# Kernel optimization log

Hardware: AMD Instinct MI355X
Metric: run time of the kernel (lower is better)

## Reference

```python
import jax, jax.numpy as jnp
import numpy as np

EPS = 1e-5
K_UP = 5      # k_upsample
SCALE = 2

def _conv(x, w, pad):
    # NCHW conv, no bias
    return jax.lax.conv_general_dilated(
        x, w, window_strides=(1, 1), padding=((pad, pad), (pad, pad)),
        dimension_numbers=('NCHW', 'OIHW', 'NCHW'))

def _bn(x, gamma, beta):
    # train-mode BatchNorm2d forward: batch stats over (N,H,W), biased var
    m = x.mean(axis=(0, 2, 3), keepdims=True)
    v = x.var(axis=(0, 2, 3), keepdims=True)
    xn = (x - m) * jax.lax.rsqrt(v + EPS)
    return xn * gamma[None, :, None, None] + beta[None, :, None, None]

def _pixel_shuffle(x, r):
    b, c, h, w = x.shape
    co = c // (r * r)
    x = x.reshape(b, co, r, r, h, w)
    x = x.transpose(0, 1, 4, 2, 5, 3)  # b, co, h, r, w, r
    return x.reshape(b, co, h * r, w * r)

def setup_inputs() -> dict:
    key = jax.random.key(0)
    ks = jax.random.split(key, 3)
    b, c, h, w = 8, 128, 64, 64
    mid = 64
    return {
        'x': jax.random.normal(ks[0], (b, c, h, w), jnp.float32),
        'comp_w': jax.random.normal(ks[1], (mid, c, 1, 1), jnp.float32) * (1.0 / np.sqrt(c)),
        'comp_g': jnp.ones((mid,), jnp.float32),
        'comp_b': jnp.zeros((mid,), jnp.float32),
        'enc_w': jax.random.normal(ks[2], ((K_UP * SCALE) ** 2, mid, 3, 3), jnp.float32) * (1.0 / np.sqrt(mid * 9)),
        'enc_g': jnp.ones(((K_UP * SCALE) ** 2,), jnp.float32),
        'enc_b': jnp.zeros(((K_UP * SCALE) ** 2,), jnp.float32),
    }

def reference(x, comp_w, comp_g, comp_b, enc_w, enc_g, enc_b):
    b, c, h, w = x.shape
    hm, wm = h * SCALE, w * SCALE
    # --- kernel prediction branch ---
    t = jax.nn.silu(_bn(_conv(x, comp_w, 0), comp_g, comp_b))        # [b,64,h,w]
    t = _bn(_conv(t, enc_w, 1), enc_g, enc_b)                        # [b,100,h,w] (act=False)
    t = _pixel_shuffle(t, SCALE)                                     # [b,25,hm,wm]
    wgt = jax.nn.softmax(t, axis=1)                                  # [b,25,hm,wm]
    # --- feature reassembly branch ---
    x_up = jnp.repeat(jnp.repeat(x, SCALE, axis=2), SCALE, axis=3)   # nearest upsample
    pad = (K_UP // 2) * SCALE  # = 4, preserves hm x wm with dilation=SCALE
    xp = jnp.pad(x_up, ((0, 0), (0, 0), (pad, pad), (pad, pad)))
    # unfold: kernel K_UP, dilation SCALE -> [b, c, 25, hm, wm], taps in (kh, kw) order
    patches = jnp.stack(
        [xp[:, :, dy * SCALE:dy * SCALE + hm, dx * SCALE:dx * SCALE + wm]
         for dy in range(K_UP) for dx in range(K_UP)], axis=2)
    # content-aware weighted sum over the 25 taps
    return jnp.einsum('bkhw,bckhw->bchw', wgt, patches)
```

## Files before the change

kernel.cpp:

```cpp
#include <hip/hip_runtime.h>
#include <hip/hip_bf16.h>
#include <math.h>

#define C_   128
#define HW_  4096
#define OC_  100
#define NSTAT_ 32768.0f

typedef __bf16 bf16x8 __attribute__((ext_vector_type(8)));
typedef __bf16 bf16x4 __attribute__((ext_vector_type(4)));
typedef float  f32x4  __attribute__((ext_vector_type(4)));

__global__ __launch_bounds__(256, 4) void k_conv1(const float* __restrict__ x,
                                                  const float* __restrict__ w,
                                                  const float* __restrict__ wenc,
                                                  __bf16* __restrict__ t1c,
                                                  float* __restrict__ csum,
                                                  float* __restrict__ csq,
                                                  __bf16* __restrict__ wprep) {
    __shared__ __bf16 xt[64 * 128];
    __shared__ __bf16 wt[64 * 128];
    __shared__ float sS[64], sQ[64];

    int blk = blockIdx.x;
    int b = blk & 7;
    int chunk = blk >> 3;
    int px0 = chunk * 64;
    int tid = threadIdx.x;
    if (tid < 64) { sS[tid] = 0.f; sQ[tid] = 0.f; }

    if (blk < 63) {
#pragma unroll
        for (int u = 0; u < 4; ++u) {
            int idx = blk * 1024 + u * 256 + tid;
            int oc = idx / 576, k = idx - oc * 576;
            int tap = k >> 6, ic = k & 63;
            wprep[idx] = (oc < OC_) ? (__bf16)wenc[((size_t)oc * 64 + ic) * 9 + tap]
                                    : (__bf16)0.f;
        }
    }

#pragma unroll
    for (int it = 0; it < 8; ++it) {
        int j = it * 256 + tid;
        int oc = j >> 5, f = j & 31;
        float4 v = *(const float4*)(w + (size_t)oc * 128 + f * 4);
        int blki = (f >> 1) ^ (oc & 15);
        bf16x4 st;
        st[0] = (__bf16)v.x; st[1] = (__bf16)v.y; st[2] = (__bf16)v.z; st[3] = (__bf16)v.w;
        *(bf16x4*)&wt[oc * 128 + blki * 8 + (f & 1) * 4] = st;
    }
#pragma unroll
    for (int it = 0; it < 2; ++it) {
        int j = it * 256 + tid;
        int px4 = (j & 15) * 4, icq = j >> 4;
        const float* xp = x + ((size_t)b * C_ + icq * 4) * HW_ + px0 + px4;
        float4 v0 = *(const float4*)(xp);
        float4 v1 = *(const float4*)(xp + HW_);
        float4 v2 = *(const float4*)(xp + 2 * HW_);
        float4 v3 = *(const float4*)(xp + 3 * HW_);
        float r0[4] = {v0.x, v0.y, v0.z, v0.w};
        float r1[4] = {v1.x, v1.y, v1.z, v1.w};
        float r2_[4] = {v2.x, v2.y, v2.z, v2.w};
        float r3[4] = {v3.x, v3.y, v3.z, v3.w};
#pragma unroll
        for (int r2 = 0; r2 < 4; ++r2) {
            int px = px4 + r2;
            int blki = (icq >> 1) ^ (px & 15);
            bf16x4 st;
            st[0] = (__bf16)r0[r2]; st[1] = (__bf16)r1[r2];
            st[2] = (__bf16)r2_[r2]; st[3] = (__bf16)r3[r2];
            *(bf16x4*)&xt[px * 128 + blki * 8 + (icq & 1) * 4] = st;
        }
    }
    __syncthreads();

    int lane = tid & 63, wv = tid >> 6;
    int p = lane & 15, q = lane >> 4;

    f32x4 acc[4];
#pragma unroll
    for (int n = 0; n < 4; ++n) acc[n] = (f32x4){0.f, 0.f, 0.f, 0.f};

#pragma unroll
    for (int kk = 0; kk < 4; ++kk) {
        int blki = (kk * 4 + q) ^ p;
        bf16x8 a = *(const bf16x8*)&xt[(wv * 16 + p) * 128 + blki * 8];
#pragma unroll
        for (int n = 0; n < 4; ++n) {
            bf16x8 bb = *(const bf16x8*)&wt[(n * 16 + p) * 128 + blki * 8];
            acc[n] = __builtin_amdgcn_mfma_f32_16x16x32_bf16(a, bb, acc[n], 0, 0, 0);
        }
    }

    __bf16* t1b = t1c + ((size_t)b * HW_ + px0 + wv * 16) * 64;
#pragma unroll
    for (int n = 0; n < 4; ++n) {
        float s = 0.f, qq = 0.f;
#pragma unroll
        for (int rg = 0; rg < 4; ++rg) {
            float v = acc[n][rg];
            t1b[(size_t)(q * 4 + rg) * 64 + n * 16 + p] = (__bf16)v;
            s += v; qq += v * v;
        }
        s += __shfl_down(s, 32, 64);  s += __shfl_down(s, 16, 64);
        qq += __shfl_down(qq, 32, 64); qq += __shfl_down(qq, 16, 64);
        if (lane < 16) {
            atomicAdd(&sS[n * 16 + p], s);
            atomicAdd(&sQ[n * 16 + p], qq);
        }
    }
    __syncthreads();
    if (tid < 64) {
        atomicAdd(&csum[tid], sS[tid]);
        atomicAdd(&csq[tid], sQ[tid]);
    }
}

__global__ __launch_bounds__(256, 4) void k_conv3(const __bf16* __restrict__ t1c,
                                                  const __bf16* __restrict__ wprep,
                                                  const float* __restrict__ csum,
                                                  const float* __restrict__ csq,
                                                  const float* __restrict__ cg,
                                                  const float* __restrict__ cb,
                                                  float* __restrict__ t2c,
                                                  float* __restrict__ esum,
                                                  float* __restrict__ esq) {
    __shared__ float shbuf[6160];
    __bf16* xt  = (__bf16*)shbuf;
    __bf16* btb = (__bf16*)((char*)shbuf + 14400);
    float*  xtf = shbuf;
    __shared__ float lsc[64], lsh[64];
    __shared__ float esuml[112], esql[112];

    int blk = blockIdx.x;
    int b = blk & 7;
    int rest = blk >> 3;
    int tile = rest & 63;
    int half = rest >> 6;
    int ty0 = (tile >> 3) * 8, tx0 = (tile & 7) * 8;
    int tid = threadIdx.x;
    const int oc0 = half * 64;
    const int NOC = half ? 48 : 64;
    const int NT  = half ? 3 : 4;

    if (tid < 112) { esuml[tid] = 0.f; esql[tid] = 0.f; }
    if (tid >= 128 && tid < 192) {
        int c = tid - 128;
        float invN = 1.0f / NSTAT_;
        float m = csum[c] * invN;
        float v = csq[c] * invN - m * m;
        float rs = rsqrtf(v + 1e-5f);
        float sc = cg[c] * rs;
        lsc[c] = sc;
        lsh[c] = cb[c] - m * sc;
    }

    int soc = tid >> 2, spart = tid & 3;
    bool sact = soc < NOC;
    int sdst = soc * 40 + spart * 8;
    const __bf16* wsrc = wprep + (size_t)(oc0 + soc) * 576 + spart * 8;

    if (sact) *(bf16x8*)&btb[sdst] = *(const bf16x8*)(wsrc);
    __syncthreads();

    const __bf16* tb = t1c + (size_t)b * HW_ * 64;
#pragma unroll
    for (int it = 0; it < 7; ++it) {
        int idx = it * 256 + tid;
        if (idx < 1600) {
            int pxi = idx >> 4, f4 = idx & 15;
            int yy = pxi / 10, xx = pxi - yy * 10;
            int gy = ty0 + yy - 1, gx = tx0 + xx - 1;
            float o0 = 0.f, o1 = 0.f, o2 = 0.f, o3 = 0.f;
            if (gy >= 0 && gy < 64 && gx >= 0 && gx < 64) {
                bf16x4 v = *(const bf16x4*)(tb + ((size_t)(gy << 6) + gx) * 64 + f4 * 4);
                float4 sc = *(const float4*)(lsc + f4 * 4);
                float4 sh = *(const float4*)(lsh + f4 * 4);
                float u;
                u = fmaf((float)v[0], sc.x, sh.x); o0 = u / (1.f + __expf(-u));
                u = fmaf((float)v[1], sc.y, sh.y); o1 = u / (1.f + __expf(-u));
                u = fmaf((float)v[2], sc.z, sh.z); o2 = u / (1.f + __expf(-u));
                u = fmaf((float)v[3], sc.w, sh.w); o3 = u / (1.f + __expf(-u));
            }
            bf16x4 st;
            st[0] = (__bf16)o0; st[1] = (__bf16)o1; st[2] = (__bf16)o2; st[3] = (__bf16)o3;
            *(bf16x4*)&xt[pxi * 72 + f4 * 4] = st;
        }
    }
    __syncthreads();

    int lane = tid & 63, wv = tid >> 6;
    int p = lane & 15, q = lane >> 4;
    int ya = 2 * wv + (p >> 3), xa = p & 7;

    f32x4 acc[4];
#pragma unroll
    for (int n = 0; n < 4; ++n) acc[n] = (f32x4){0.f, 0.f, 0.f, 0.f};

#pragma unroll
    for (int kk = 0; kk < 18; ++kk) {
        const int cur = kk & 1;
        bf16x8 r0;
        if (kk < 17 && sact) r0 = *(const bf16x8*)(wsrc + (kk + 1) * 32);
        const int tap = kk >> 1, ich = (kk & 1) * 32;
        const int ky = tap / 3, kx = tap - ky * 3;
        bf16x8 a0 = *(const bf16x8*)&xt[((ya + ky) * 10 + xa + kx) * 72 + ich + q * 8];
        const __bf16* btc = btb + cur * 2560;
#pragma unroll
        for (int n = 0; n < 4; ++n) {
            if (n < NT) {
                bf16x8 bb = *(const bf16x8*)&btc[(n * 16 + p) * 40 + q * 8];
                acc[n] = __builtin_amdgcn_mfma_f32_16x16x32_bf16(a0, bb, acc[n], 0, 0, 0);
            }
        }
        if (kk < 17) {
            if (sact) *(bf16x8*)&btb[(1 - cur) * 2560 + sdst] = r0;
            __syncthreads();
        }
    }
    __syncthreads();

#pragma unroll
    for (int n = 0; n < 4; ++n) {
        if (n < NT) {
            int ocl = n * 16 + p;
            int oc = oc0 + ocl;
            int k5l = ocl >> 2, sch = ocl & 3;
            bool wr = oc < OC_;
            float s = 0.f, qq = 0.f;
#pragma unroll
            for (int rg = 0; rg < 4; ++rg) {
                int mp = q * 4 + rg;
                float v = acc[n][rg];
                if (wr) xtf[k5l * 260 + (2 * wv + (mp >> 3)) * 32 + (mp & 7) * 4 + sch] = v;
                s += v; qq += v * v;
            }
            s += __shfl_down(s, 32, 64);  s += __shfl_down(s, 16, 64);
            qq += __shfl_down(qq, 32, 64); qq += __shfl_down(qq, 16, 64);
            if (lane < 16) {
                atomicAdd(&esuml[oc0 + n * 16 + lane], s);
                atomicAdd(&esql[oc0 + n * 16 + lane], qq);
            }
        }
    }
    __syncthreads();

    const int NK5 = half ? 9 : 16;
    const int jobs = NK5 * 64;
    float* t2b = t2c + (size_t)b * 25 * HW_ * 4;
#pragma unroll
    for (int it = 0; it < 4; ++it) {
        int idx = it * 256 + tid;
        if (idx < jobs) {
            int k5l = idx >> 6, pix = idx & 63;
            f32x4 v = *(const f32x4*)&xtf[k5l * 260 + pix * 4];
            int gy = ty0 + (pix >> 3), gx = tx0 + (pix & 7);
            *(f32x4*)&t2b[((size_t)(half * 16 + k5l) * HW_ + (gy << 6) + gx) * 4] = v;
        }
    }
    if (tid >= oc0 && tid < oc0 + NOC) {
        atomicAdd(&esum[tid], esuml[tid]);
        atomicAdd(&esq[tid], esql[tid]);
    }
}

__global__ __launch_bounds__(512, 2) void k_carafe(const float* __restrict__ x,
                                                   const float* __restrict__ t2c,
                                                   const float* __restrict__ esum,
                                                   const float* __restrict__ esq,
                                                   const float* __restrict__ eg,
                                                   const float* __restrict__ eb,
                                                   float* __restrict__ out) {
    __shared__ float xt[400 * 20];
    __shared__ float esc[112], esh[112];

    int blk = blockIdx.x;
    int b = blk & 7;
    int r = blk >> 3;
    int tile = r & 15;
    int cq = r >> 4;
    int tx0 = (tile & 3) * 16, ty0 = (tile >> 2) * 16;
    int tid = threadIdx.x;
    if (tid < 112) {
        float invN = 1.0f / NSTAT_;
        float m = esum[tid] * invN;
        float v = esq[tid] * invN - m * m;
        float rs = rsqrtf(v + 1e-5f);
        float sc = (tid < OC_) ? eg[tid] * rs : 0.f;
        esc[tid] = sc;
        esh[tid] = (tid < OC_) ? eb[tid] - m * sc : 0.f;
    }

    int t0 = tid & 1, px = tid >> 1;
    int pxx = px & 15, py = px >> 4;
    int iy = ty0 + py, jx = tx0 + pxx;
    int pxl = (iy << 6) + jx;

    const float* xb = x + (size_t)b * C_ * HW_;

    f32x4 pf[4];
#pragma unroll
    for (int it = 0; it < 4; ++it) {
        int idx = it * 512 + tid;
        if (idx < 1600) {
            int c4 = idx / 400;
            int hp = idx - c4 * 400;
            int yy = hp / 20, xx = hp - yy * 20;
            int gy = ty0 - 2 + yy, gx = tx0 - 2 + xx;
            f32x4 st = {0.f, 0.f, 0.f, 0.f};
            if (gy >= 0 && gy < 64 && gx >= 0 && gx < 64) {
                size_t base = (size_t)(cq * 32 + c4 * 4) * HW_ + (gy << 6) + gx;
                st[0] = xb[base];
                st[1] = xb[base + HW_];
                st[2] = xb[base + 2 * HW_];
                st[3] = xb[base + 3 * HW_];
            }
            pf[it] = st;
        }
    }
    __syncthreads();

    float wA[25], wB[25];
    {
        const float* t2p = t2c + (size_t)b * 25 * HW_ * 4 + (size_t)pxl * 4 + 2 * t0;
        int cA = 2 * t0, cB = 2 * t0 + 1;
        float mxA = -1e30f, mxB = -1e30f;
#pragma unroll
        for (int k = 0; k < 25; ++k) {
            float2 v = *(const float2*)(t2p + (size_t)k * HW_ * 4);
            float lA = fmaf(v.x, esc[4 * k + cA], esh[4 * k + cA]);
            float lB = fmaf(v.y, esc[4 * k + cB], esh[4 * k + cB]);
            wA[k] = lA; wB[k] = lB;
            mxA = fmaxf(mxA, lA); mxB = fmaxf(mxB, lB);
        }
        float sA = 0.f, sB = 0.f;
#pragma unroll
        for (int k = 0; k < 25; ++k) {
            float eA = __expf(wA[k] - mxA);
            float eB = __expf(wB[k] - mxB);
            wA[k] = eA; wB[k] = eB;
            sA += eA; sB += eB;
        }
        float iA = 1.f / sA, iB = 1.f / sB;
#pragma unroll
        for (int k = 0; k < 25; ++k) { wA[k] *= iA; wB[k] *= iB; }
    }

#pragma unroll
    for (int it = 0; it < 4; ++it) {
        int idx = it * 512 + tid;
        if (idx < 1600) {
            int c4 = idx / 400;
            int hp = idx - c4 * 400;
            *(f32x4*)&xt[hp * 20 + c4 * 4] = pf[it];
        }
    }
    __syncthreads();

    int i0 = iy * 2 + t0;
    float* op = out + (size_t)b * C_ * 16384 + (size_t)i0 * 128 + jx * 2;
    int cbase = cq * 32;

    f32x4 pg[4];
#pragma unroll
    for (int it = 0; it < 4; ++it) {
        int idx = it * 512 + tid;
        if (idx < 1600) {
            int c4 = idx / 400;
            int hp = idx - c4 * 400;
            int yy = hp / 20, xx = hp - yy * 20;
            int gy = ty0 - 2 + yy, gx = tx0 - 2 + xx;
            f32x4 st = {0.f, 0.f, 0.f, 0.f};
            if (gy >= 0 && gy < 64 && gx >= 0 && gx < 64) {
                size_t base = (size_t)(cbase + 16 + c4 * 4) * HW_ + (gy << 6) + gx;
                st[0] = xb[base];
                st[1] = xb[base + HW_];
                st[2] = xb[base + 2 * HW_];
                st[3] = xb[base + 3 * HW_];
            }
            pg[it] = st;
        }
    }

    {
        float accA[16], accB[16];
#pragma unroll
        for (int e = 0; e < 16; ++e) { accA[e] = 0.f; accB[e] = 0.f; }
#pragma unroll
        for (int dy = 0; dy < 5; ++dy)
#pragma unroll
            for (int dx = 0; dx < 5; ++dx) {
                int pos = (py + dy) * 20 + pxx + dx;
                float a = wA[dy * 5 + dx], bw = wB[dy * 5 + dx];
#pragma unroll
                for (int c4 = 0; c4 < 4; ++c4) {
                    f32x4 xv = *(const f32x4*)&xt[pos * 20 + c4 * 4];
                    accA[c4 * 4 + 0] = fmaf(a, xv[0], accA[c4 * 4 + 0]);
                    accA[c4 * 4 + 1] = fmaf(a, xv[1], accA[c4 * 4 + 1]);
                    accA[c4 * 4 + 2] = fmaf(a, xv[2], accA[c4 * 4 + 2]);
                    accA[c4 * 4 + 3] = fmaf(a, xv[3], accA[c4 * 4 + 3]);
                    accB[c4 * 4 + 0] = fmaf(bw, xv[0], accB[c4 * 4 + 0]);
                    accB[c4 * 4 + 1] = fmaf(bw, xv[1], accB[c4 * 4 + 1]);
                    accB[c4 * 4 + 2] = fmaf(bw, xv[2], accB[c4 * 4 + 2]);
                    accB[c4 * 4 + 3] = fmaf(bw, xv[3], accB[c4 * 4 + 3]);
                }
            }
#pragma unroll
        for (int e = 0; e < 16; ++e) {
            float2 st2;
            st2.x = accA[e]; st2.y = accB[e];
            *(float2*)&op[(size_t)(cbase + e) * 16384] = st2;
        }
    }
    __syncthreads();

#pragma unroll
    for (int it = 0; it < 4; ++it) {
        int idx = it * 512 + tid;
        if (idx < 1600) {
            int c4 = idx / 400;
            int hp = idx - c4 * 400;
            *(f32x4*)&xt[hp * 20 + c4 * 4] = pg[it];
        }
    }
    __syncthreads();

    {
        float accA[16], accB[16];
#pragma unroll
        for (int e = 0; e < 16; ++e) { accA[e] = 0.f; accB[e] = 0.f; }
#pragma unroll
        for (int dy = 0; dy < 5; ++dy)
#pragma unroll
            for (int dx = 0; dx < 5; ++dx) {
                int pos = (py + dy) * 20 + pxx + dx;
                float a = wA[dy * 5 + dx], bw = wB[dy * 5 + dx];
#pragma unroll
                for (int c4 = 0; c4 < 4; ++c4) {
                    f32x4 xv = *(const f32x4*)&xt[pos * 20 + c4 * 4];
                    accA[c4 * 4 + 0] = fmaf(a, xv[0], accA[c4 * 4 + 0]);
                    accA[c4 * 4 + 1] = fmaf(a, xv[1], accA[c4 * 4 + 1]);
                    accA[c4 * 4 + 2] = fmaf(a, xv[2], accA[c4 * 4 + 2]);
                    accA[c4 * 4 + 3] = fmaf(a, xv[3], accA[c4 * 4 + 3]);
                    accB[c4 * 4 + 0] = fmaf(bw, xv[0], accB[c4 * 4 + 0]);
                    accB[c4 * 4 + 1] = fmaf(bw, xv[1], accB[c4 * 4 + 1]);
                    accB[c4 * 4 + 2] = fmaf(bw, xv[2], accB[c4 * 4 + 2]);
                    accB[c4 * 4 + 3] = fmaf(bw, xv[3], accB[c4 * 4 + 3]);
                }
            }
#pragma unroll
        for (int e = 0; e < 16; ++e) {
            float2 st2;
            st2.x = accA[e]; st2.y = accB[e];
            *(float2*)&op[(size_t)(cbase + 16 + e) * 16384] = st2;
        }
    }
}

extern "C" void kernel_launch(void* const* d_in, const int* in_sizes, int n_in,
                              void* d_out, int out_size, void* d_ws, size_t ws_size,
                              hipStream_t stream) {
    const float* x      = (const float*)d_in[0];
    const float* comp_w = (const float*)d_in[1];
    const float* comp_g = (const float*)d_in[2];
    const float* comp_b = (const float*)d_in[3];
    const float* enc_w  = (const float*)d_in[4];
    const float* enc_g  = (const float*)d_in[5];
    const float* enc_b  = (const float*)d_in[6];
    float* out = (float*)d_out;

    float* ws = (float*)d_ws;
    __bf16* t1c = (__bf16*)ws;
    float* t2c  = ws + 1048576;
    float* st   = ws + 1048576 + 3670016;
    float* csum = st;
    float* csq  = st + 64;
    float* esum = st + 128;
    float* esq  = st + 240;
    __bf16* wprep = (__bf16*)(st + 352);

    hipMemsetAsync(st, 0, 352 * sizeof(float), stream);
    k_conv1<<<512, 256, 0, stream>>>(x, comp_w, enc_w, t1c, csum, csq, wprep);
    k_conv3<<<1024, 256, 0, stream>>>(t1c, wprep, csum, csq, comp_g, comp_b, t2c, esum, esq);
    k_carafe<<<512, 512, 0, stream>>>(x, t2c, esum, esq, enc_g, enc_b, out);
}
```

Baseline: 158.6 us.

## Halve conv1 pixel tile and stage full 3x3 taps per barrier in conv3

conv1 now handles 32 pixels per block and launches twice as many blocks, with each wave computing a 16x32 sub-tile so all four waves split the output channels. conv3 stages one whole tap (64 input channels) of weights per double-buffer step instead of half a tap, which halves the number of __syncthreads in the K loop at the cost of more shared memory. The smaller conv1 tile aims to improve occupancy and latency hiding, but it re-reads the conv1 weights per block and doubles the atomics on the stats.

```diff
diff --git a/kernel.cpp b/kernel.cpp
--- a/kernel.cpp
+++ b/kernel.cpp
@@ -18,14 +18,14 @@
                                                   float* __restrict__ csum,
                                                   float* __restrict__ csq,
                                                   __bf16* __restrict__ wprep) {
-    __shared__ __bf16 xt[64 * 128];
+    __shared__ __bf16 xt[32 * 128];
     __shared__ __bf16 wt[64 * 128];
     __shared__ float sS[64], sQ[64];
 
     int blk = blockIdx.x;
     int b = blk & 7;
     int chunk = blk >> 3;
-    int px0 = chunk * 64;
+    int px0 = chunk * 32;
     int tid = threadIdx.x;
     if (tid < 64) { sS[tid] = 0.f; sQ[tid] = 0.f; }
 
@@ -50,10 +50,9 @@
         st[0] = (__bf16)v.x; st[1] = (__bf16)v.y; st[2] = (__bf16)v.z; st[3] = (__bf16)v.w;
         *(bf16x4*)&wt[oc * 128 + blki * 8 + (f & 1) * 4] = st;
     }
-#pragma unroll
-    for (int it = 0; it < 2; ++it) {
-        int j = it * 256 + tid;
-        int px4 = (j & 15) * 4, icq = j >> 4;
+    {
+        int j = tid;
+        int px4 = (j & 7) * 4, icq = j >> 3;
         const float* xp = x + ((size_t)b * C_ + icq * 4) * HW_ + px0 + px4;
         float4 v0 = *(const float4*)(xp);
         float4 v1 = *(const float4*)(xp + HW_);
@@ -77,37 +76,40 @@
 
     int lane = tid & 63, wv = tid >> 6;
     int p = lane & 15, q = lane >> 4;
-
-    f32x4 acc[4];
-#pragma unroll
-    for (int n = 0; n < 4; ++n) acc[n] = (f32x4){0.f, 0.f, 0.f, 0.f};
+    int mrow = (wv & 1) * 16;
+    int nbase = (wv >> 1) * 2;
+
+    f32x4 acc[2];
+#pragma unroll
+    for (int n = 0; n < 2; ++n) acc[n] = (f32x4){0.f, 0.f, 0.f, 0.f};
 
 #pragma unroll
     for (int kk = 0; kk < 4; ++kk) {
         int blki = (kk * 4 + q) ^ p;
-        bf16x8 a = *(const bf16x8*)&xt[(wv * 16 + p) * 128 + blki * 8];
-#pragma unroll
-        for (int n = 0; n < 4; ++n) {
-            bf16x8 bb = *(const bf16x8*)&wt[(n * 16 + p) * 128 + blki * 8];
+        bf16x8 a = *(const bf16x8*)&xt[(mrow + p) * 128 + blki * 8];
+#pragma unroll
+        for (int n = 0; n < 2; ++n) {
+            bf16x8 bb = *(const bf16x8*)&wt[((nbase + n) * 16 + p) * 128 + blki * 8];
             acc[n] = __builtin_amdgcn_mfma_f32_16x16x32_bf16(a, bb, acc[n], 0, 0, 0);
         }
     }
 
-    __bf16* t1b = t1c + ((size_t)b * HW_ + px0 + wv * 16) * 64;
-#pragma unroll
-    for (int n = 0; n < 4; ++n) {
+    __bf16* t1b = t1c + ((size_t)b * HW_ + px0 + mrow) * 64;
+#pragma unroll
+    for (int n = 0; n < 2; ++n) {
+        int ch = (nbase + n) * 16 + p;
         float s = 0.f, qq = 0.f;
 #pragma unroll
         for (int rg = 0; rg < 4; ++rg) {
             float v = acc[n][rg];
-            t1b[(size_t)(q * 4 + rg) * 64 + n * 16 + p] = (__bf16)v;
+            t1b[(size_t)(q * 4 + rg) * 64 + ch] = (__bf16)v;
             s += v; qq += v * v;
         }
         s += __shfl_down(s, 32, 64);  s += __shfl_down(s, 16, 64);
         qq += __shfl_down(qq, 32, 64); qq += __shfl_down(qq, 16, 64);
         if (lane < 16) {
-            atomicAdd(&sS[n * 16 + p], s);
-            atomicAdd(&sQ[n * 16 + p], qq);
+            atomicAdd(&sS[ch], s);
+            atomicAdd(&sQ[ch], qq);
         }
     }
     __syncthreads();
@@ -126,7 +128,7 @@
                                                   float* __restrict__ t2c,
                                                   float* __restrict__ esum,
                                                   float* __restrict__ esq) {
-    __shared__ float shbuf[6160];
+    __shared__ float shbuf[8208];
     __bf16* xt  = (__bf16*)shbuf;
     __bf16* btb = (__bf16*)((char*)shbuf + 14400);
     float*  xtf = shbuf;
@@ -158,10 +160,13 @@
 
     int soc = tid >> 2, spart = tid & 3;
     bool sact = soc < NOC;
-    int sdst = soc * 40 + spart * 8;
+    int sdst = soc * 72 + spart * 8;
     const __bf16* wsrc = wprep + (size_t)(oc0 + soc) * 576 + spart * 8;
 
-    if (sact) *(bf16x8*)&btb[sdst] = *(const bf16x8*)(wsrc);
+    if (sact) {
+        *(bf16x8*)&btb[sdst]      = *(const bf16x8*)(wsrc);
+        *(bf16x8*)&btb[sdst + 32] = *(const bf16x8*)(wsrc + 32);
+    }
     __syncthreads();
 
     const __bf16* tb = t1c + (size_t)b * HW_ * 64;
@@ -199,23 +204,32 @@
     for (int n = 0; n < 4; ++n) acc[n] = (f32x4){0.f, 0.f, 0.f, 0.f};
 
 #pragma unroll
-    for (int kk = 0; kk < 18; ++kk) {
-        const int cur = kk & 1;
-        bf16x8 r0;
-        if (kk < 17 && sact) r0 = *(const bf16x8*)(wsrc + (kk + 1) * 32);
-        const int tap = kk >> 1, ich = (kk & 1) * 32;
+    for (int tap = 0; tap < 9; ++tap) {
+        const int cur = tap & 1;
+        bf16x8 r0, r1;
+        if (tap < 8 && sact) {
+            r0 = *(const bf16x8*)(wsrc + (tap + 1) * 64);
+            r1 = *(const bf16x8*)(wsrc + (tap + 1) * 64 + 32);
+        }
         const int ky = tap / 3, kx = tap - ky * 3;
-        bf16x8 a0 = *(const bf16x8*)&xt[((ya + ky) * 10 + xa + kx) * 72 + ich + q * 8];
-        const __bf16* btc = btb + cur * 2560;
-#pragma unroll
-        for (int n = 0; n < 4; ++n) {
-            if (n < NT) {
-                bf16x8 bb = *(const bf16x8*)&btc[(n * 16 + p) * 40 + q * 8];
-                acc[n] = __builtin_amdgcn_mfma_f32_16x16x32_bf16(a0, bb, acc[n], 0, 0, 0);
-            }
-        }
-        if (kk < 17) {
-            if (sact) *(bf16x8*)&btb[(1 - cur) * 2560 + sdst] = r0;
+        const __bf16* btc = btb + cur * 4608;
+        const int arow = ((ya + ky) * 10 + xa + kx) * 72;
+#pragma unroll
+        for (int ich2 = 0; ich2 < 2; ++ich2) {
+            bf16x8 a0 = *(const bf16x8*)&xt[arow + ich2 * 32 + q * 8];
+#pragma unroll
+            for (int n = 0; n < 4; ++n) {
+                if (n < NT) {
+                    bf16x8 bb = *(const bf16x8*)&btc[(n * 16 + p) * 72 + ich2 * 32 + q * 8];
+                    acc[n] = __builtin_amdgcn_mfma_f32_16x16x32_bf16(a0, bb, acc[n], 0, 0, 0);
+                }
+            }
+        }
+        if (tap < 8) {
+            if (sact) {
+                *(bf16x8*)&btb[(1 - cur) * 4608 + sdst]      = r0;
+                *(bf16x8*)&btb[(1 - cur) * 4608 + sdst + 32] = r1;
+            }
             __syncthreads();
         }
     }
@@ -481,7 +495,7 @@
     __bf16* wprep = (__bf16*)(st + 352);
 
     hipMemsetAsync(st, 0, 352 * sizeof(float), stream);
-    k_conv1<<<512, 256, 0, stream>>>(x, comp_w, enc_w, t1c, csum, csq, wprep);
+    k_conv1<<<1024, 256, 0, stream>>>(x, comp_w, enc_w, t1c, csum, csq, wprep);
     k_conv3<<<1024, 256, 0, stream>>>(t1c, wprep, csum, csq, comp_g, comp_b, t2c, esum, esq);
     k_carafe<<<512, 512, 0, stream>>>(x, t2c, esum, esq, enc_g, enc_b, out);
 }
```

Measured after the change: 170.6 us. 1.08x slower.
